# Performance work log

Hardware: AMD Instinct MI355X
Metric: run time of the kernel (lower is better)

The kernel has to match this reference:

```python
import jax, jax.numpy as jnp
import numpy as np

B, N, D, E, H = 8, 256, 128, 32, 4
HD = D // H
EPS = 1e-5


def setup_inputs() -> dict:
    key = jax.random.key(0)
    ks = jax.random.split(key, 20)
    idx = jnp.arange(N)

    h = jax.random.normal(ks[0], (B, N, D), dtype=jnp.float32)
    adj = (jax.random.uniform(ks[1], (B, N, N)) < 0.5).astype(jnp.float32)
    adj = adj.at[:, idx, idx].set(1.0)
    edge_features = jax.random.normal(ks[2], (B, N, N, E), dtype=jnp.float32)
    src_mask = (jax.random.uniform(ks[3], (B, N, N)) < 0.7).astype(jnp.float32)
    src_mask = src_mask.at[:, idx, idx].set(1.0)

    s = 1.0 / np.sqrt(D)
    se = 1.0 / np.sqrt(E)
    p = {
        "gcn_w": jax.random.normal(ks[4], (D, D)) * s,
        "gcn_b": jnp.zeros((D,)),
        "edge_w": jax.random.normal(ks[5], (D, E)) * se,
        "edge_b": jnp.zeros((D,)),
        "wq": jax.random.normal(ks[6], (D, D)) * s,
        "wk": jax.random.normal(ks[7], (D, D)) * s,
        "wv": jax.random.normal(ks[8], (D, D)) * s,
        "bq": jnp.zeros((D,)),
        "bk": jnp.zeros((D,)),
        "bv": jnp.zeros((D,)),
        "out_w": jax.random.normal(ks[9], (D, D)) * s,
        "out_b": jnp.zeros((D,)),
        "ln_g": jnp.ones((D,)),
        "ln_b": jnp.zeros((D,)),
    }
    return {"h": h, "adj": adj, "edge_features": edge_features, "src_mask": src_mask, **p}


def reference(h, adj, edge_features, src_mask,
              gcn_w, gcn_b, edge_w, edge_b,
              wq, wk, wv, bq, bk, bv, out_w, out_b, ln_g, ln_b):
    b, n, d = h.shape

    # --- GCN branch: degree-normalized aggregation with self-loops ---
    adj_sl = adj + jnp.eye(n, dtype=h.dtype)[None]          # (B,N,N)
    deg = adj_sl.sum(-1, keepdims=True)                      # (B,N,1)
    h_agg = jnp.einsum('bnm,bmd->bnd', adj_sl, h) / deg
    h_gcn = h_agg @ gcn_w.T + gcn_b                          # (B,N,D)

    # --- edge-conditioned key/value: h_ij = h_j + edge_emb ---
    edge_emb = jnp.einsum('bnme,de->bnmd', edge_features, edge_w) + edge_b
    h_ij = h[:, None, :, :] + edge_emb                       # (B,N,N,D)

    # key padding mask: True where edge absent (masked)
    masked = (adj * src_mask) == 0                           # (B,N,N)

    # --- multi-head attention, one query per node ---
    q = (h @ wq.T + bq).reshape(b, n, H, HD)                 # (B,N,H,HD)
    k = (jnp.einsum('bnmd,ed->bnme', h_ij, wk) + bk).reshape(b, n, n, H, HD)
    v = (jnp.einsum('bnmd,ed->bnme', h_ij, wv) + bv).reshape(b, n, n, H, HD)

    scores = jnp.einsum('bnhd,bnmhd->bnhm', q, k) / np.sqrt(HD)  # (B,N,H,N)
    scores = jnp.where(masked[:, :, None, :], -jnp.inf, scores)
    attn = jax.nn.softmax(scores, axis=-1)
    o = jnp.einsum('bnhm,bnmhd->bnhd', attn, v).reshape(b, n, d)
    o = o @ out_w.T + out_b                                  # (B,N,D)

    # residual + layernorm (dropout is identity in eval)
    x = h + o
    mu = x.mean(-1, keepdims=True)
    var = ((x - mu) ** 2).mean(-1, keepdims=True)
    h_attn = ln_g * (x - mu) / jnp.sqrt(var + EPS) + ln_b

    return h_gcn + h_attn
```

## Files before the change

### kernel.cpp

```cpp
#include <hip/hip_runtime.h>
#include <hip/hip_bf16.h>

#define OFF_WQT 0
#define OFF_WKT 16384
#define OFF_WVT 32768
#define OFF_OWT 49152
#define OFF_GWT 65536
#define OFF_WKE 81920
#define OFF_WVET 86016
#define OFF_KB  90112
#define OFF_VB  90240
#define OFF_SC  90368
#define OFF_QS  98560
#define OFF_QE  360704
#define OFF_HG  622848
#define OFF_K0  884992
#define OFF_V0  1016064

static __device__ __forceinline__ float bflo(unsigned int w){
  union { unsigned int u; float f; } x; x.u = w << 16; return x.f;
}
static __device__ __forceinline__ float bfhi(unsigned int w){
  union { unsigned int u; float f; } x; x.u = w & 0xffff0000u; return x.f;
}
static __device__ __forceinline__ unsigned int f2bf(float f){
  union { float f; unsigned int u; } x; x.f = f;
  return (x.u + 0x7fffu + ((x.u >> 16) & 1u)) >> 16;
}

__global__ __launch_bounds__(256) void prep_kernel(
    const float* __restrict__ wq, const float* __restrict__ wk,
    const float* __restrict__ wv, const float* __restrict__ out_w,
    const float* __restrict__ gcn_w, const float* __restrict__ edge_w,
    const float* __restrict__ edge_b, const float* __restrict__ bk,
    const float* __restrict__ bv, float* __restrict__ ws)
{
  int blk = blockIdx.x, t = threadIdx.x;
  if (blk < 320) {
    int w = blk >> 6;
    int e0 = (blk & 63) * 256 + t;
    const float* src = (w==0) ? wq : (w==1) ? wk : (w==2) ? wv : (w==3) ? out_w : gcn_w;
    float* dst = ws + ((w==0) ? OFF_WQT : (w==1) ? OFF_WKT : (w==2) ? OFF_WVT
                      : (w==3) ? OFF_OWT : OFF_GWT);
    int k = e0 >> 7, d = e0 & 127;
    dst[e0] = src[d*128 + k];
  } else if (blk < 352) {
    int idx = blk - 320;
    int which = idx >> 4;
    int e0 = (idx & 15) * 256 + t;
    int dd = e0 >> 5, e = e0 & 31;
    const float* W = which ? wv : wk;
    float acc = 0.f;
    #pragma unroll 4
    for (int k2 = 0; k2 < 128; ++k2) acc += W[dd*128+k2] * edge_w[k2*32+e];
    if (which) ws[OFF_WVET + e*128 + dd] = acc;
    else       ws[OFF_WKE + e0] = acc;
  } else {
    int dd = t & 127;
    const float* W  = (t < 128) ? wk : wv;
    const float* bb = (t < 128) ? bk : bv;
    float acc = bb[dd];
    #pragma unroll 4
    for (int k2 = 0; k2 < 128; ++k2) acc += W[dd*128+k2] * edge_b[k2];
    ws[((t < 128) ? OFF_KB : OFF_VB) + dd] = acc;
  }
}

__global__ __launch_bounds__(256) void proj_kernel(
    const float* __restrict__ h, const float* __restrict__ adj,
    const float* __restrict__ bq, const float* __restrict__ gcn_b,
    float* __restrict__ ws)
{
  __shared__ float h_lds[256];
  __shared__ float adj_lds[512];
  __shared__ float p1[2][2][128];
  __shared__ float p2[2][2][128];
  __shared__ float p3[2][2][128];
  __shared__ float qrow[2*132];
  __shared__ float dpart[2][2];
  __shared__ float ha_lds[2*132];

  int t = threadIdx.x;
  int d = t & 127, kh = t >> 7;
  int r0 = blockIdx.x * 2;
  int b  = r0 >> 8, n0 = r0 & 255;

  if (t < 64)  ((float4*)h_lds)[t]   = ((const float4*)(h   + (size_t)r0*128))[t];
  if (t < 128) ((float4*)adj_lds)[t] = ((const float4*)(adj + (size_t)r0*256))[t];
  __syncthreads();

  {
    const float* wqT = ws + OFF_WQT;
    const float* wkT = ws + OFF_WKT;
    const float* wvT = ws + OFF_WVT;
    float aq0=0,aq1=0,ak0=0,ak1=0,av0=0,av1=0;
    #pragma unroll 4
    for (int kk = 0; kk < 64; ++kk) {
      int k = kh*64 + kk;
      float qw = wqT[k*128+d], kw = wkT[k*128+d], vw = wvT[k*128+d];
      float h0 = h_lds[k], h1 = h_lds[128+k];
      aq0 += qw*h0; aq1 += qw*h1;
      ak0 += kw*h0; ak1 += kw*h1;
      av0 += vw*h0; av1 += vw*h1;
    }
    p1[kh][0][d]=aq0; p1[kh][1][d]=aq1;
    p2[kh][0][d]=ak0; p2[kh][1][d]=ak1;
    p3[kh][0][d]=av0; p3[kh][1][d]=av1;
  }
  __syncthreads();

  {
    unsigned short* K0 = (unsigned short*)(ws + OFF_K0);
    unsigned short* V0 = (unsigned short*)(ws + OFF_V0);
    int i = t >> 7, dd = t & 127;
    const float inv = 0.17677669529663687f;
    float q = (p1[0][i][dd] + p1[1][i][dd] + bq[dd]) * inv;
    ws[OFF_QS + (size_t)(r0+i)*128 + dd] = q;
    qrow[i*132 + dd] = q;
    K0[(size_t)(r0+i)*128 + dd] = (unsigned short)f2bf(p2[0][i][dd] + p2[1][i][dd]);
    V0[(size_t)(r0+i)*128 + dd] = (unsigned short)f2bf(p3[0][i][dd] + p3[1][i][dd]);
  }
  __syncthreads();

  {
    float ag0=0, ag1=0, dg0=0, dg1=0;
    #pragma unroll 4
    for (int mm = 0; mm < 128; ++mm) {
      int ml = kh*128 + mm;
      float hv = h[((size_t)b*256 + ml)*128 + d];
      float a0 = adj_lds[ml]       + ((ml == n0)     ? 1.0f : 0.0f);
      float a1 = adj_lds[256 + ml] + ((ml == n0 + 1) ? 1.0f : 0.0f);
      ag0 += a0*hv; ag1 += a1*hv; dg0 += a0; dg1 += a1;
    }
    p1[kh][0][d]=ag0; p1[kh][1][d]=ag1;
    if (d == 0) { dpart[kh][0]=dg0; dpart[kh][1]=dg1; }
  }
  {
    int i = t >> 7, he = t & 127, hh = he >> 5, e = he & 31;
    float acc = 0.f;
    #pragma unroll
    for (int j = 0; j < 32; ++j)
      acc += ws[OFF_WKE + (hh*32 + j)*32 + e] * qrow[i*132 + hh*32 + j];
    ws[OFF_QE + (size_t)(r0+i)*128 + he] = acc;
  }
  if (t < 8) {
    int i = t >> 2, hh = t & 3;
    float acc = 0.f;
    #pragma unroll
    for (int j = 0; j < 32; ++j)
      acc += qrow[i*132 + hh*32 + j] * ws[OFF_KB + hh*32 + j];
    ws[OFF_SC + (size_t)(r0+i)*4 + hh] = acc;
  }
  __syncthreads();

  {
    int i = t >> 7, dd = t & 127;
    ha_lds[i*132 + dd] = (p1[0][i][dd] + p1[1][i][dd]) / (dpart[0][i] + dpart[1][i]);
  }
  __syncthreads();

  {
    const float* gwT = ws + OFF_GWT;
    float g0=0, g1=0;
    #pragma unroll 4
    for (int kk = 0; kk < 64; ++kk) {
      int k = kh*64 + kk;
      float gw = gwT[k*128+d];
      g0 += gw * ha_lds[k];
      g1 += gw * ha_lds[132 + k];
    }
    p2[kh][0][d]=g0; p2[kh][1][d]=g1;
  }
  __syncthreads();
  {
    int i = t >> 7, dd = t & 127;
    ws[OFF_HG + (size_t)(r0+i)*128 + dd] = p2[0][i][dd] + p2[1][i][dd] + gcn_b[dd];
  }
}

__global__ __launch_bounds__(256, 4) void attn_kernel(
    const float* __restrict__ edge, const float* __restrict__ adj,
    const float* __restrict__ srcm, const float* __restrict__ h,
    const float* __restrict__ out_b, const float* __restrict__ ln_g,
    const float* __restrict__ ln_b, const float* __restrict__ ws,
    float* __restrict__ out)
{
  __shared__ unsigned int e_bf[256*18];
  __shared__ float s_lds[4*264];
  __shared__ float part4[8*132];
  __shared__ float part5[8*132];
  __shared__ float qs_l[132];
  __shared__ float qe_l[132];
  __shared__ float sc_l[4];
  __shared__ float ebar[128];
  __shared__ float wpart[16];
  __shared__ float red[2];

  int t  = threadIdx.x;
  int bn = blockIdx.x;
  int b  = bn >> 8;

  {
    const float4* et = (const float4*)(edge + (size_t)bn*8192);
    #pragma unroll
    for (int it = 0; it < 8; ++it) {
      int fi = it*256 + t;
      float4 v = et[fi];
      int row = fi >> 3, c4 = fi & 7;
      uint2 pk;
      pk.x = f2bf(v.x) | (f2bf(v.y) << 16);
      pk.y = f2bf(v.z) | (f2bf(v.w) << 16);
      *(uint2*)(e_bf + row*18 + c4*2) = pk;
    }
    float mp = adj[(size_t)bn*256 + t] * srcm[(size_t)bn*256 + t];
    e_bf[t*18 + 16] = __float_as_uint(mp);
    if (t < 128) {
      int hh = t >> 5, j = t & 31;
      qs_l[hh*33 + j] = ws[OFF_QS + (size_t)bn*128 + t];
      qe_l[hh*33 + j] = ws[OFF_QE + (size_t)bn*128 + t];
    }
    if (t < 4) sc_l[t] = ws[OFF_SC + (size_t)bn*4 + t];
  }
  __syncthreads();

  int hh = t & 3;
  {
    const float* qp  = qs_l + hh*33;
    const float* qep = qe_l + hh*33;
    float exsum = 0.f;
    const unsigned short* K0 = (const unsigned short*)(ws + OFF_K0) + (size_t)b*256*128;
    #pragma unroll 2
    for (int pass = 0; pass < 4; ++pass) {
      int mm = (pass << 6) | (t >> 2);
      const uint4* kv = (const uint4*)(K0 + (size_t)mm*128) + hh*4;
      float acc = sc_l[hh];
      #pragma unroll
      for (int q4 = 0; q4 < 4; ++q4) {
        uint4 kw = kv[q4];
        const float* qq = qp + q4*8;
        acc += qq[0]*bflo(kw.x) + qq[1]*bfhi(kw.x)
             + qq[2]*bflo(kw.y) + qq[3]*bfhi(kw.y)
             + qq[4]*bflo(kw.z) + qq[5]*bfhi(kw.z)
             + qq[6]*bflo(kw.w) + qq[7]*bfhi(kw.w);
      }
      const uint2* er = (const uint2*)(e_bf + mm*18);
      #pragma unroll
      for (int j = 0; j < 8; ++j) {
        uint2 w = er[j];
        acc += qep[4*j+0]*bflo(w.x) + qep[4*j+1]*bfhi(w.x)
             + qep[4*j+2]*bflo(w.y) + qep[4*j+3]*bfhi(w.y);
      }
      float mp = __uint_as_float(e_bf[mm*18 + 16]);
      float ex = (mp == 0.0f) ? 0.0f : __expf(acc);
      s_lds[hh*264 + mm] = ex;
      exsum += ex;
    }
    exsum += __shfl_down(exsum, 4);
    exsum += __shfl_down(exsum, 8);
    exsum += __shfl_down(exsum, 16);
    exsum += __shfl_down(exsum, 32);
    if ((t & 63) < 4) wpart[(t >> 6)*4 + hh] = exsum;
  }
  __syncthreads();

  {
    float s0 = wpart[0]+wpart[4]+wpart[8]+wpart[12];
    float s1 = wpart[1]+wpart[5]+wpart[9]+wpart[13];
    float s2h = wpart[2]+wpart[6]+wpart[10]+wpart[14];
    float s3h = wpart[3]+wpart[7]+wpart[11]+wpart[15];

    int ms  = t >> 5;
    int hh4 = (t >> 3) & 3, e4 = t & 7;
    int c   = t & 31,  hh5 = c >> 3;
    float sum4 = (hh4==0)?s0:(hh4==1)?s1:(hh4==2)?s2h:s3h;
    float sum5 = (hh5==0)?s0:(hh5==1)?s1:(hh5==2)?s2h:s3h;
    float inv4 = 1.0f / sum4, inv5 = 1.0f / sum5;

    float p4x=0,p4y=0,p4z=0,p4w=0;
    float p5x=0,p5y=0,p5z=0,p5w=0;
    const unsigned int* vrow = (const unsigned int*)(ws + OFF_V0) + (size_t)b*256*64;
    for (int jm = 0; jm < 32; ++jm) {
      int mm = ms*32 + jm;
      float a4 = s_lds[hh4*264 + mm];
      uint2 w = *(const uint2*)(e_bf + mm*18 + e4*2);
      p4x += a4*bflo(w.x); p4y += a4*bfhi(w.x);
      p4z += a4*bflo(w.y); p4w += a4*bfhi(w.y);
      float a5 = s_lds[hh5*264 + mm];
      uint2 vv = *(const uint2*)(vrow + (size_t)mm*64 + c*2);
      p5x += a5*bflo(vv.x); p5y += a5*bfhi(vv.x);
      p5z += a5*bflo(vv.y); p5w += a5*bfhi(vv.y);
    }
    float4 f4; f4.x=p4x*inv4; f4.y=p4y*inv4; f4.z=p4z*inv4; f4.w=p4w*inv4;
    *(float4*)(part4 + ms*132 + hh4*32 + e4*4) = f4;
    float4 f5; f5.x=p5x*inv5; f5.y=p5y*inv5; f5.z=p5z*inv5; f5.w=p5w*inv5;
    *(float4*)(part5 + ms*132 + c*4) = f5;
  }
  __syncthreads();

  float s2 = 0.f;
  if (t < 128) {
    float se = 0.f;
    #pragma unroll
    for (int g = 0; g < 8; ++g) { se += part4[g*132 + t]; s2 += part5[g*132 + t]; }
    ebar[t] = se;
  }
  __syncthreads();

  float hv = 0.f;
  if (t < 128) {
    int hd = t >> 5;
    float acc = s2 + ws[OFF_VB + t];
    const float* wveT = ws + OFF_WVET;
    #pragma unroll 4
    for (int e = 0; e < 32; ++e) acc += wveT[e*128 + t] * ebar[hd*32 + e];
    part4[t] = acc;
    hv = h[(size_t)bn*128 + t];
  }
  __syncthreads();

  float x = 0.f;
  if (t < 128) {
    const float* owT = ws + OFF_OWT;
    float acc = out_b[t] + hv;
    #pragma unroll 8
    for (int k = 0; k < 128; ++k) acc += owT[k*128 + t] * part4[k];
    x = acc;
    part4[132 + t] = x;
  }
  __syncthreads();

  if (t < 64) {
    float x0 = part4[132 + t], x1 = part4[132 + t + 64];
    float s = x0 + x1, ss = x0*x0 + x1*x1;
    #pragma unroll
    for (int off = 32; off > 0; off >>= 1) {
      s  += __shfl_down(s,  off);
      ss += __shfl_down(ss, off);
    }
    if (t == 0) {
      float mu = s * (1.0f/128.0f);
      red[0] = mu;
      red[1] = rsqrtf(ss * (1.0f/128.0f) - mu*mu + 1e-5f);
    }
  }
  __syncthreads();

  if (t < 128) {
    float mu = red[0], rs = red[1];
    out[(size_t)bn*128 + t] =
        ln_g[t]*(x - mu)*rs + ln_b[t] + ws[OFF_HG + (size_t)bn*128 + t];
  }
}

extern "C" void kernel_launch(void* const* d_in, const int* in_sizes, int n_in,
                              void* d_out, int out_size, void* d_ws, size_t ws_size,
                              hipStream_t stream) {
  (void)in_sizes; (void)n_in; (void)out_size; (void)ws_size;
  const float* h     = (const float*)d_in[0];
  const float* adj   = (const float*)d_in[1];
  const float* edge  = (const float*)d_in[2];
  const float* srcm  = (const float*)d_in[3];
  const float* gcn_w = (const float*)d_in[4];
  const float* gcn_b = (const float*)d_in[5];
  const float* edge_w= (const float*)d_in[6];
  const float* edge_b= (const float*)d_in[7];
  const float* wq    = (const float*)d_in[8];
  const float* wk    = (const float*)d_in[9];
  const float* wv    = (const float*)d_in[10];
  const float* bq    = (const float*)d_in[11];
  const float* bk    = (const float*)d_in[12];
  const float* bv    = (const float*)d_in[13];
  const float* out_w = (const float*)d_in[14];
  const float* out_b = (const float*)d_in[15];
  const float* ln_g  = (const float*)d_in[16];
  const float* ln_b  = (const float*)d_in[17];

  float* ws  = (float*)d_ws;
  float* out = (float*)d_out;

  prep_kernel<<<353, 256, 0, stream>>>(wq, wk, wv, out_w, gcn_w, edge_w, edge_b, bk, bv, ws);
  proj_kernel<<<1024, 256, 0, stream>>>(h, adj, bq, gcn_b, ws);
  attn_kernel<<<2048, 256, 0, stream>>>(edge, adj, srcm, h, out_b, ln_g, ln_b, ws, out);
}
```

Measured before the change: 189.0 us.

## Tile attention over keys with fp32 K/V and register-prefetched edge features

```diff
diff --git a/kernel.cpp b/kernel.cpp
--- a/kernel.cpp
+++ b/kernel.cpp
@@ -14,19 +14,8 @@
 #define OFF_QS  98560
 #define OFF_QE  360704
 #define OFF_HG  622848
-#define OFF_K0  884992
-#define OFF_V0  1016064
-
-static __device__ __forceinline__ float bflo(unsigned int w){
-  union { unsigned int u; float f; } x; x.u = w << 16; return x.f;
-}
-static __device__ __forceinline__ float bfhi(unsigned int w){
-  union { unsigned int u; float f; } x; x.u = w & 0xffff0000u; return x.f;
-}
-static __device__ __forceinline__ unsigned int f2bf(float f){
-  union { float f; unsigned int u; } x; x.f = f;
-  return (x.u + 0x7fffu + ((x.u >> 16) & 1u)) >> 16;
-}
+#define OFF_KF  884992
+#define OFF_VF  1147136
 
 __global__ __launch_bounds__(256) void prep_kernel(
     const float* __restrict__ wq, const float* __restrict__ wk,
@@ -110,15 +99,13 @@
   __syncthreads();
 
   {
-    unsigned short* K0 = (unsigned short*)(ws + OFF_K0);
-    unsigned short* V0 = (unsigned short*)(ws + OFF_V0);
     int i = t >> 7, dd = t & 127;
     const float inv = 0.17677669529663687f;
     float q = (p1[0][i][dd] + p1[1][i][dd] + bq[dd]) * inv;
     ws[OFF_QS + (size_t)(r0+i)*128 + dd] = q;
     qrow[i*132 + dd] = q;
-    K0[(size_t)(r0+i)*128 + dd] = (unsigned short)f2bf(p2[0][i][dd] + p2[1][i][dd]);
-    V0[(size_t)(r0+i)*128 + dd] = (unsigned short)f2bf(p3[0][i][dd] + p3[1][i][dd]);
+    ws[OFF_KF + (size_t)(r0+i)*128 + dd] = p2[0][i][dd] + p2[1][i][dd];
+    ws[OFF_VF + (size_t)(r0+i)*128 + dd] = p3[0][i][dd] + p3[1][i][dd];
   }
   __syncthreads();
 
@@ -178,142 +165,152 @@
   }
 }
 
-__global__ __launch_bounds__(256, 4) void attn_kernel(
+__global__ __launch_bounds__(256) void attn_kernel(
     const float* __restrict__ edge, const float* __restrict__ adj,
     const float* __restrict__ srcm, const float* __restrict__ h,
     const float* __restrict__ out_b, const float* __restrict__ ln_g,
     const float* __restrict__ ln_b, const float* __restrict__ ws,
     float* __restrict__ out)
 {
-  __shared__ unsigned int e_bf[256*18];
-  __shared__ float s_lds[4*264];
+  __shared__ float e_lds[64*34];
+  __shared__ float s_lds[4*68];
+  __shared__ float mp_lds[256];
+  __shared__ float qs_l[132];
+  __shared__ float sc_l[4];
   __shared__ float part4[8*132];
   __shared__ float part5[8*132];
-  __shared__ float qs_l[132];
-  __shared__ float qe_l[132];
-  __shared__ float sc_l[4];
-  __shared__ float ebar[128];
+  __shared__ float ebar_l[128];
+  __shared__ float o_l[128];
+  __shared__ float x_l[128];
   __shared__ float wpart[16];
   __shared__ float red[2];
 
-  int t  = threadIdx.x;
-  int bn = blockIdx.x;
-  int b  = bn >> 8;
-
-  {
-    const float4* et = (const float4*)(edge + (size_t)bn*8192);
-    #pragma unroll
-    for (int it = 0; it < 8; ++it) {
-      int fi = it*256 + t;
-      float4 v = et[fi];
-      int row = fi >> 3, c4 = fi & 7;
-      uint2 pk;
-      pk.x = f2bf(v.x) | (f2bf(v.y) << 16);
-      pk.y = f2bf(v.z) | (f2bf(v.w) << 16);
-      *(uint2*)(e_bf + row*18 + c4*2) = pk;
-    }
-    float mp = adj[(size_t)bn*256 + t] * srcm[(size_t)bn*256 + t];
-    e_bf[t*18 + 16] = __float_as_uint(mp);
-    if (t < 128) {
-      int hh = t >> 5, j = t & 31;
-      qs_l[hh*33 + j] = ws[OFF_QS + (size_t)bn*128 + t];
-      qe_l[hh*33 + j] = ws[OFF_QE + (size_t)bn*128 + t];
-    }
-    if (t < 4) sc_l[t] = ws[OFF_SC + (size_t)bn*4 + t];
-  }
-  __syncthreads();
-
-  int hh = t & 3;
-  {
-    const float* qp  = qs_l + hh*33;
-    const float* qep = qe_l + hh*33;
-    float exsum = 0.f;
-    const unsigned short* K0 = (const unsigned short*)(ws + OFF_K0) + (size_t)b*256*128;
-    #pragma unroll 2
-    for (int pass = 0; pass < 4; ++pass) {
-      int mm = (pass << 6) | (t >> 2);
-      const uint4* kv = (const uint4*)(K0 + (size_t)mm*128) + hh*4;
+  const int t  = threadIdx.x;
+  const int bn = blockIdx.x;
+  const int b  = bn >> 8;
+  const int hh = t & 3;
+  const int mq = t >> 2;
+  const int c  = t & 31;
+  const int ms = t >> 5;
+
+  float qe_r[4][8];
+  {
+    const float* qeg = ws + OFF_QE + (size_t)bn*128 + hh*8;
+    #pragma unroll
+    for (int hp = 0; hp < 4; ++hp) {
+      float4 a = *(const float4*)(qeg + hp*32);
+      float4 d2 = *(const float4*)(qeg + hp*32 + 4);
+      qe_r[hp][0]=a.x;  qe_r[hp][1]=a.y;  qe_r[hp][2]=a.z;  qe_r[hp][3]=a.w;
+      qe_r[hp][4]=d2.x; qe_r[hp][5]=d2.y; qe_r[hp][6]=d2.z; qe_r[hp][7]=d2.w;
+    }
+  }
+  mp_lds[t] = adj[(size_t)bn*256 + t] * srcm[(size_t)bn*256 + t];
+  if (t < 128) qs_l[(t>>5)*33 + (t&31)] = ws[OFF_QS + (size_t)bn*128 + t];
+  if (t < 4)  sc_l[t] = ws[OFF_SC + (size_t)bn*4 + t];
+
+  const float* eg = edge + (size_t)bn*8192;
+  float4 eA = *(const float4*)(eg + t*8);
+  float4 eB = *(const float4*)(eg + t*8 + 4);
+
+  const float* K0f = ws + OFF_KF + (size_t)b*32768;
+  const float* V0f = ws + OFF_VF + (size_t)b*32768;
+
+  float exacc = 0.f;
+  float p4x=0,p4y=0,p4z=0,p4w=0, p5x=0,p5y=0,p5z=0,p5w=0;
+
+  __syncthreads();
+
+  float4 eA2 = eA, eB2 = eB;
+  for (int tile = 0; tile < 4; ++tile) {
+    {
+      float* dst = e_lds + mq*34 + hh*8;
+      float2 w0; w0.x=eA.x; w0.y=eA.y; *(float2*)(dst+0)=w0;
+      float2 w1; w1.x=eA.z; w1.y=eA.w; *(float2*)(dst+2)=w1;
+      float2 w2; w2.x=eB.x; w2.y=eB.y; *(float2*)(dst+4)=w2;
+      float2 w3; w3.x=eB.z; w3.y=eB.w; *(float2*)(dst+6)=w3;
+    }
+    {
+      const float* qp = qs_l + hh*33;
+      const float4* kv = (const float4*)(K0f + (size_t)(tile*64 + mq)*128 + hh*32);
       float acc = sc_l[hh];
       #pragma unroll
-      for (int q4 = 0; q4 < 4; ++q4) {
-        uint4 kw = kv[q4];
-        const float* qq = qp + q4*8;
-        acc += qq[0]*bflo(kw.x) + qq[1]*bfhi(kw.x)
-             + qq[2]*bflo(kw.y) + qq[3]*bfhi(kw.y)
-             + qq[4]*bflo(kw.z) + qq[5]*bfhi(kw.z)
-             + qq[6]*bflo(kw.w) + qq[7]*bfhi(kw.w);
+      for (int q4 = 0; q4 < 8; ++q4) {
+        float4 kw = kv[q4];
+        const float* qq = qp + q4*4;
+        acc += qq[0]*kw.x + qq[1]*kw.y + qq[2]*kw.z + qq[3]*kw.w;
       }
-      const uint2* er = (const uint2*)(e_bf + mm*18);
-      #pragma unroll
-      for (int j = 0; j < 8; ++j) {
-        uint2 w = er[j];
-        acc += qep[4*j+0]*bflo(w.x) + qep[4*j+1]*bfhi(w.x)
-             + qep[4*j+2]*bflo(w.y) + qep[4*j+3]*bfhi(w.y);
-      }
-      float mp = __uint_as_float(e_bf[mm*18 + 16]);
+      float es0 = eA.x*qe_r[0][0]+eA.y*qe_r[0][1]+eA.z*qe_r[0][2]+eA.w*qe_r[0][3]
+                + eB.x*qe_r[0][4]+eB.y*qe_r[0][5]+eB.z*qe_r[0][6]+eB.w*qe_r[0][7];
+      float es1 = eA.x*qe_r[1][0]+eA.y*qe_r[1][1]+eA.z*qe_r[1][2]+eA.w*qe_r[1][3]
+                + eB.x*qe_r[1][4]+eB.y*qe_r[1][5]+eB.z*qe_r[1][6]+eB.w*qe_r[1][7];
+      float es2 = eA.x*qe_r[2][0]+eA.y*qe_r[2][1]+eA.z*qe_r[2][2]+eA.w*qe_r[2][3]
+                + eB.x*qe_r[2][4]+eB.y*qe_r[2][5]+eB.z*qe_r[2][6]+eB.w*qe_r[2][7];
+      float es3 = eA.x*qe_r[3][0]+eA.y*qe_r[3][1]+eA.z*qe_r[3][2]+eA.w*qe_r[3][3]
+                + eB.x*qe_r[3][4]+eB.y*qe_r[3][5]+eB.z*qe_r[3][6]+eB.w*qe_r[3][7];
+      es0 += __shfl_xor(es0, 1); es0 += __shfl_xor(es0, 2);
+      es1 += __shfl_xor(es1, 1); es1 += __shfl_xor(es1, 2);
+      es2 += __shfl_xor(es2, 1); es2 += __shfl_xor(es2, 2);
+      es3 += __shfl_xor(es3, 1); es3 += __shfl_xor(es3, 2);
+      acc += (hh==0) ? es0 : (hh==1) ? es1 : (hh==2) ? es2 : es3;
+      float mp = mp_lds[tile*64 + mq];
       float ex = (mp == 0.0f) ? 0.0f : __expf(acc);
-      s_lds[hh*264 + mm] = ex;
-      exsum += ex;
-    }
-    exsum += __shfl_down(exsum, 4);
-    exsum += __shfl_down(exsum, 8);
-    exsum += __shfl_down(exsum, 16);
-    exsum += __shfl_down(exsum, 32);
-    if ((t & 63) < 4) wpart[(t >> 6)*4 + hh] = exsum;
-  }
-  __syncthreads();
-
-  {
-    float s0 = wpart[0]+wpart[4]+wpart[8]+wpart[12];
-    float s1 = wpart[1]+wpart[5]+wpart[9]+wpart[13];
-    float s2h = wpart[2]+wpart[6]+wpart[10]+wpart[14];
-    float s3h = wpart[3]+wpart[7]+wpart[11]+wpart[15];
-
-    int ms  = t >> 5;
-    int hh4 = (t >> 3) & 3, e4 = t & 7;
-    int c   = t & 31,  hh5 = c >> 3;
-    float sum4 = (hh4==0)?s0:(hh4==1)?s1:(hh4==2)?s2h:s3h;
-    float sum5 = (hh5==0)?s0:(hh5==1)?s1:(hh5==2)?s2h:s3h;
-    float inv4 = 1.0f / sum4, inv5 = 1.0f / sum5;
-
-    float p4x=0,p4y=0,p4z=0,p4w=0;
-    float p5x=0,p5y=0,p5z=0,p5w=0;
-    const unsigned int* vrow = (const unsigned int*)(ws + OFF_V0) + (size_t)b*256*64;
-    for (int jm = 0; jm < 32; ++jm) {
-      int mm = ms*32 + jm;
-      float a4 = s_lds[hh4*264 + mm];
-      uint2 w = *(const uint2*)(e_bf + mm*18 + e4*2);
-      p4x += a4*bflo(w.x); p4y += a4*bfhi(w.x);
-      p4z += a4*bflo(w.y); p4w += a4*bfhi(w.y);
-      float a5 = s_lds[hh5*264 + mm];
-      uint2 vv = *(const uint2*)(vrow + (size_t)mm*64 + c*2);
-      p5x += a5*bflo(vv.x); p5y += a5*bfhi(vv.x);
-      p5z += a5*bflo(vv.y); p5w += a5*bfhi(vv.y);
-    }
-    float4 f4; f4.x=p4x*inv4; f4.y=p4y*inv4; f4.z=p4z*inv4; f4.w=p4w*inv4;
-    *(float4*)(part4 + ms*132 + hh4*32 + e4*4) = f4;
-    float4 f5; f5.x=p5x*inv5; f5.y=p5y*inv5; f5.z=p5z*inv5; f5.w=p5w*inv5;
+      s_lds[hh*68 + mq] = ex;
+      exacc += ex;
+    }
+    if (tile < 3) {
+      eA2 = *(const float4*)(eg + (tile+1)*2048 + t*8);
+      eB2 = *(const float4*)(eg + (tile+1)*2048 + t*8 + 4);
+    }
+    __syncthreads();
+
+    #pragma unroll
+    for (int jm = 0; jm < 8; ++jm) {
+      int mm = ms*8 + jm;
+      float a = s_lds[(c>>3)*68 + mm];
+      float2 e0 = *(const float2*)(e_lds + mm*34 + (c&7)*4);
+      float2 e1 = *(const float2*)(e_lds + mm*34 + (c&7)*4 + 2);
+      float4 vv = *(const float4*)(V0f + (size_t)(tile*64 + mm)*128 + c*4);
+      p4x += a*e0.x; p4y += a*e0.y; p4z += a*e1.x; p4w += a*e1.y;
+      p5x += a*vv.x; p5y += a*vv.y; p5z += a*vv.z; p5w += a*vv.w;
+    }
+    __syncthreads();
+    eA = eA2; eB = eB2;
+  }
+
+  {
+    float s = exacc;
+    s += __shfl_down(s, 4);  s += __shfl_down(s, 8);
+    s += __shfl_down(s, 16); s += __shfl_down(s, 32);
+    if ((t & 63) < 4) wpart[(t >> 6)*4 + hh] = s;
+  }
+  {
+    float4 f4; f4.x=p4x; f4.y=p4y; f4.z=p4z; f4.w=p4w;
+    *(float4*)(part4 + ms*132 + c*4) = f4;
+    float4 f5; f5.x=p5x; f5.y=p5y; f5.z=p5z; f5.w=p5w;
     *(float4*)(part5 + ms*132 + c*4) = f5;
   }
   __syncthreads();
 
   float s2 = 0.f;
   if (t < 128) {
+    int ht = t >> 5;
+    float inv = 1.0f / (wpart[ht] + wpart[4+ht] + wpart[8+ht] + wpart[12+ht]);
     float se = 0.f;
     #pragma unroll
     for (int g = 0; g < 8; ++g) { se += part4[g*132 + t]; s2 += part5[g*132 + t]; }
-    ebar[t] = se;
+    ebar_l[t] = se * inv;
+    s2 *= inv;
   }
   __syncthreads();
 
   float hv = 0.f;
   if (t < 128) {
-    int hd = t >> 5;
+    int ht = t >> 5;
     float acc = s2 + ws[OFF_VB + t];
     const float* wveT = ws + OFF_WVET;
     #pragma unroll 4
-    for (int e = 0; e < 32; ++e) acc += wveT[e*128 + t] * ebar[hd*32 + e];
-    part4[t] = acc;
+    for (int e = 0; e < 32; ++e) acc += wveT[e*128 + t] * ebar_l[ht*32 + e];
+    o_l[t] = acc;
     hv = h[(size_t)bn*128 + t];
   }
   __syncthreads();
@@ -323,14 +320,14 @@
     const float* owT = ws + OFF_OWT;
     float acc = out_b[t] + hv;
     #pragma unroll 8
-    for (int k = 0; k < 128; ++k) acc += owT[k*128 + t] * part4[k];
+    for (int k = 0; k < 128; ++k) acc += owT[k*128 + t] * o_l[k];
     x = acc;
-    part4[132 + t] = x;
+    x_l[t] = x;
   }
   __syncthreads();
 
   if (t < 64) {
-    float x0 = part4[132 + t], x1 = part4[132 + t + 64];
+    float x0 = x_l[t], x1 = x_l[t + 64];
     float s = x0 + x1, ss = x0*x0 + x1*x1;
     #pragma unroll
     for (int off = 32; off > 0; off >>= 1) {
@@ -346,9 +343,8 @@
   __syncthreads();
 
   if (t < 128) {
-    float mu = red[0], rs = red[1];
     out[(size_t)bn*128 + t] =
-        ln_g[t]*(x - mu)*rs + ln_b[t] + ws[OFF_HG + (size_t)bn*128 + t];
+        ln_g[t]*(x - red[0])*red[1] + ln_b[t] + ws[OFF_HG + (size_t)bn*128 + t];
   }
 }
 
```

After: 258.2 us. +36.6%, slower.

## Switch attention operands to fp16 packed dot2 and split epilogue into batched kernel

Applied to the files above, without the earlier changes.

```diff
diff --git a/kernel.cpp b/kernel.cpp
--- a/kernel.cpp
+++ b/kernel.cpp
@@ -11,21 +11,26 @@
 #define OFF_KB  90112
 #define OFF_VB  90240
 #define OFF_SC  90368
-#define OFF_QS  98560
-#define OFF_QE  360704
-#define OFF_HG  622848
-#define OFF_K0  884992
-#define OFF_V0  1016064
-
-static __device__ __forceinline__ float bflo(unsigned int w){
-  union { unsigned int u; float f; } x; x.u = w << 16; return x.f;
-}
-static __device__ __forceinline__ float bfhi(unsigned int w){
-  union { unsigned int u; float f; } x; x.u = w & 0xffff0000u; return x.f;
-}
-static __device__ __forceinline__ unsigned int f2bf(float f){
-  union { float f; unsigned int u; } x; x.f = f;
-  return (x.u + 0x7fffu + ((x.u >> 16) & 1u)) >> 16;
+#define OFF_QSP 98560
+#define OFF_QEP 229632
+#define OFF_HG  360704
+#define OFF_EB  622848
+#define OFF_OV  884992
+#define OFF_K0P 1147136
+#define OFF_V0P 1278208
+
+using half2_t = __attribute__((ext_vector_type(2))) __fp16;
+
+static __device__ __forceinline__ half2_t u2h(unsigned int u){
+  union { unsigned int u; half2_t h; } x; x.u = u; return x.h;
+}
+static __device__ __forceinline__ unsigned int pkf16(float a, float b){
+  union { half2_t h; unsigned int u; } x;
+  x.h = __builtin_amdgcn_cvt_pkrtz(a, b);
+  return x.u;
+}
+static __device__ __forceinline__ float fdot2(unsigned int a, unsigned int b, float c){
+  return __builtin_amdgcn_fdot2(u2h(a), u2h(b), c, false);
 }
 
 __global__ __launch_bounds__(256) void prep_kernel(
@@ -77,6 +82,7 @@
   __shared__ float p2[2][2][128];
   __shared__ float p3[2][2][128];
   __shared__ float qrow[2*132];
+  __shared__ float qe_l[2*132];
   __shared__ float dpart[2][2];
   __shared__ float ha_lds[2*132];
 
@@ -84,6 +90,7 @@
   int d = t & 127, kh = t >> 7;
   int r0 = blockIdx.x * 2;
   int b  = r0 >> 8, n0 = r0 & 255;
+  unsigned int* wsu = (unsigned int*)ws;
 
   if (t < 64)  ((float4*)h_lds)[t]   = ((const float4*)(h   + (size_t)r0*128))[t];
   if (t < 128) ((float4*)adj_lds)[t] = ((const float4*)(adj + (size_t)r0*256))[t];
@@ -110,18 +117,44 @@
   __syncthreads();
 
   {
-    unsigned short* K0 = (unsigned short*)(ws + OFF_K0);
-    unsigned short* V0 = (unsigned short*)(ws + OFF_V0);
     int i = t >> 7, dd = t & 127;
     const float inv = 0.17677669529663687f;
-    float q = (p1[0][i][dd] + p1[1][i][dd] + bq[dd]) * inv;
-    ws[OFF_QS + (size_t)(r0+i)*128 + dd] = q;
-    qrow[i*132 + dd] = q;
-    K0[(size_t)(r0+i)*128 + dd] = (unsigned short)f2bf(p2[0][i][dd] + p2[1][i][dd]);
-    V0[(size_t)(r0+i)*128 + dd] = (unsigned short)f2bf(p3[0][i][dd] + p3[1][i][dd]);
-  }
-  __syncthreads();
-
+    qrow[i*132 + dd] = (p1[0][i][dd] + p1[1][i][dd] + bq[dd]) * inv;
+  }
+  {
+    int i = (t >> 6) & 1, pr = t & 63;
+    if (t < 128) {
+      float k0 = p2[0][i][2*pr] + p2[1][i][2*pr];
+      float k1 = p2[0][i][2*pr+1] + p2[1][i][2*pr+1];
+      wsu[OFF_K0P + (size_t)(r0+i)*64 + pr] = pkf16(k0, k1);
+    } else {
+      float v0 = p3[0][i][2*pr] + p3[1][i][2*pr];
+      float v1 = p3[0][i][2*pr+1] + p3[1][i][2*pr+1];
+      wsu[OFF_V0P + (size_t)(r0+i)*64 + pr] = pkf16(v0, v1);
+    }
+  }
+  __syncthreads();
+
+  if (t < 128) {
+    int i = t >> 6, pr = t & 63;
+    wsu[OFF_QSP + (size_t)(r0+i)*64 + pr] = pkf16(qrow[i*132 + 2*pr], qrow[i*132 + 2*pr+1]);
+  }
+  {
+    int i = t >> 7, he = t & 127, hh = he >> 5, e = he & 31;
+    float acc = 0.f;
+    #pragma unroll
+    for (int j = 0; j < 32; ++j)
+      acc += ws[OFF_WKE + (hh*32 + j)*32 + e] * qrow[i*132 + hh*32 + j];
+    qe_l[i*132 + he] = acc;
+  }
+  if (t < 8) {
+    int i = t >> 2, hh = t & 3;
+    float acc = 0.f;
+    #pragma unroll
+    for (int j = 0; j < 32; ++j)
+      acc += qrow[i*132 + hh*32 + j] * ws[OFF_KB + hh*32 + j];
+    ws[OFF_SC + (size_t)(r0+i)*4 + hh] = acc;
+  }
   {
     float ag0=0, ag1=0, dg0=0, dg1=0;
     #pragma unroll 4
@@ -135,24 +168,12 @@
     p1[kh][0][d]=ag0; p1[kh][1][d]=ag1;
     if (d == 0) { dpart[kh][0]=dg0; dpart[kh][1]=dg1; }
   }
-  {
-    int i = t >> 7, he = t & 127, hh = he >> 5, e = he & 31;
-    float acc = 0.f;
-    #pragma unroll
-    for (int j = 0; j < 32; ++j)
-      acc += ws[OFF_WKE + (hh*32 + j)*32 + e] * qrow[i*132 + hh*32 + j];
-    ws[OFF_QE + (size_t)(r0+i)*128 + he] = acc;
-  }
-  if (t < 8) {
-    int i = t >> 2, hh = t & 3;
-    float acc = 0.f;
-    #pragma unroll
-    for (int j = 0; j < 32; ++j)
-      acc += qrow[i*132 + hh*32 + j] * ws[OFF_KB + hh*32 + j];
-    ws[OFF_SC + (size_t)(r0+i)*4 + hh] = acc;
-  }
-  __syncthreads();
-
+  __syncthreads();
+
+  if (t < 128) {
+    int i = t >> 6, pr = t & 63;
+    wsu[OFF_QEP + (size_t)(r0+i)*64 + pr] = pkf16(qe_l[i*132 + 2*pr], qe_l[i*132 + 2*pr+1]);
+  }
   {
     int i = t >> 7, dd = t & 127;
     ha_lds[i*132 + dd] = (p1[0][i][dd] + p1[1][i][dd]) / (dpart[0][i] + dpart[1][i]);
@@ -180,25 +201,21 @@
 
 __global__ __launch_bounds__(256, 4) void attn_kernel(
     const float* __restrict__ edge, const float* __restrict__ adj,
-    const float* __restrict__ srcm, const float* __restrict__ h,
-    const float* __restrict__ out_b, const float* __restrict__ ln_g,
-    const float* __restrict__ ln_b, const float* __restrict__ ws,
-    float* __restrict__ out)
+    const float* __restrict__ srcm, const float* __restrict__ ws,
+    float* __restrict__ dummy)
 {
-  __shared__ unsigned int e_bf[256*18];
+  __shared__ unsigned int e_lds[256*18];
   __shared__ float s_lds[4*264];
   __shared__ float part4[8*132];
   __shared__ float part5[8*132];
-  __shared__ float qs_l[132];
-  __shared__ float qe_l[132];
-  __shared__ float sc_l[4];
-  __shared__ float ebar[128];
   __shared__ float wpart[16];
-  __shared__ float red[2];
-
-  int t  = threadIdx.x;
-  int bn = blockIdx.x;
-  int b  = bn >> 8;
+
+  const int t  = threadIdx.x;
+  const int bn = blockIdx.x;
+  const int b  = bn >> 8;
+  const int hh = t & 3;
+  const int mq = t >> 2;
+  const unsigned int* wsu = (const unsigned int*)ws;
 
   {
     const float4* et = (const float4*)(edge + (size_t)bn*8192);
@@ -208,147 +225,184 @@
       float4 v = et[fi];
       int row = fi >> 3, c4 = fi & 7;
       uint2 pk;
-      pk.x = f2bf(v.x) | (f2bf(v.y) << 16);
-      pk.y = f2bf(v.z) | (f2bf(v.w) << 16);
-      *(uint2*)(e_bf + row*18 + c4*2) = pk;
+      pk.x = pkf16(v.x, v.y);
+      pk.y = pkf16(v.z, v.w);
+      *(uint2*)(e_lds + row*18 + c4*2) = pk;
     }
     float mp = adj[(size_t)bn*256 + t] * srcm[(size_t)bn*256 + t];
-    e_bf[t*18 + 16] = __float_as_uint(mp);
-    if (t < 128) {
-      int hh = t >> 5, j = t & 31;
-      qs_l[hh*33 + j] = ws[OFF_QS + (size_t)bn*128 + t];
-      qe_l[hh*33 + j] = ws[OFF_QE + (size_t)bn*128 + t];
-    }
-    if (t < 4) sc_l[t] = ws[OFF_SC + (size_t)bn*4 + t];
-  }
-  __syncthreads();
-
-  int hh = t & 3;
-  {
-    const float* qp  = qs_l + hh*33;
-    const float* qep = qe_l + hh*33;
-    float exsum = 0.f;
-    const unsigned short* K0 = (const unsigned short*)(ws + OFF_K0) + (size_t)b*256*128;
-    #pragma unroll 2
+    e_lds[t*18 + 16] = __float_as_uint(mp);
+  }
+  unsigned int qs_pk[16], qe_pk[16];
+  {
+    const uint4* qp = (const uint4*)(wsu + OFF_QSP + (size_t)bn*64 + hh*16);
+    const uint4* qe = (const uint4*)(wsu + OFF_QEP + (size_t)bn*64 + hh*16);
+    #pragma unroll
+    for (int j = 0; j < 4; ++j) {
+      uint4 a = qp[j];
+      qs_pk[4*j+0]=a.x; qs_pk[4*j+1]=a.y; qs_pk[4*j+2]=a.z; qs_pk[4*j+3]=a.w;
+      uint4 c = qe[j];
+      qe_pk[4*j+0]=c.x; qe_pk[4*j+1]=c.y; qe_pk[4*j+2]=c.z; qe_pk[4*j+3]=c.w;
+    }
+  }
+  float sconst = ws[OFF_SC + (size_t)bn*4 + hh];
+  __syncthreads();
+
+  float exacc = 0.f;
+  {
+    const unsigned int* K0 = wsu + OFF_K0P + (size_t)b*256*64;
     for (int pass = 0; pass < 4; ++pass) {
-      int mm = (pass << 6) | (t >> 2);
-      const uint4* kv = (const uint4*)(K0 + (size_t)mm*128) + hh*4;
-      float acc = sc_l[hh];
+      int mm = (pass << 6) | mq;
+      float acc = sconst;
+      const uint4* kr4 = (const uint4*)(K0 + (size_t)mm*64 + hh*16);
       #pragma unroll
-      for (int q4 = 0; q4 < 4; ++q4) {
-        uint4 kw = kv[q4];
-        const float* qq = qp + q4*8;
-        acc += qq[0]*bflo(kw.x) + qq[1]*bfhi(kw.x)
-             + qq[2]*bflo(kw.y) + qq[3]*bfhi(kw.y)
-             + qq[4]*bflo(kw.z) + qq[5]*bfhi(kw.z)
-             + qq[6]*bflo(kw.w) + qq[7]*bfhi(kw.w);
+      for (int j4 = 0; j4 < 4; ++j4) {
+        uint4 kw = kr4[j4];
+        acc = fdot2(qs_pk[4*j4+0], kw.x, acc);
+        acc = fdot2(qs_pk[4*j4+1], kw.y, acc);
+        acc = fdot2(qs_pk[4*j4+2], kw.z, acc);
+        acc = fdot2(qs_pk[4*j4+3], kw.w, acc);
       }
-      const uint2* er = (const uint2*)(e_bf + mm*18);
+      const uint2* er = (const uint2*)(e_lds + mm*18);
       #pragma unroll
-      for (int j = 0; j < 8; ++j) {
-        uint2 w = er[j];
-        acc += qep[4*j+0]*bflo(w.x) + qep[4*j+1]*bfhi(w.x)
-             + qep[4*j+2]*bflo(w.y) + qep[4*j+3]*bfhi(w.y);
+      for (int j2 = 0; j2 < 8; ++j2) {
+        uint2 w = er[j2];
+        acc = fdot2(qe_pk[2*j2+0], w.x, acc);
+        acc = fdot2(qe_pk[2*j2+1], w.y, acc);
       }
-      float mp = __uint_as_float(e_bf[mm*18 + 16]);
+      float mp = __uint_as_float(e_lds[mm*18 + 16]);
       float ex = (mp == 0.0f) ? 0.0f : __expf(acc);
       s_lds[hh*264 + mm] = ex;
-      exsum += ex;
-    }
-    exsum += __shfl_down(exsum, 4);
-    exsum += __shfl_down(exsum, 8);
-    exsum += __shfl_down(exsum, 16);
-    exsum += __shfl_down(exsum, 32);
-    if ((t & 63) < 4) wpart[(t >> 6)*4 + hh] = exsum;
-  }
-  __syncthreads();
-
-  {
-    float s0 = wpart[0]+wpart[4]+wpart[8]+wpart[12];
-    float s1 = wpart[1]+wpart[5]+wpart[9]+wpart[13];
-    float s2h = wpart[2]+wpart[6]+wpart[10]+wpart[14];
-    float s3h = wpart[3]+wpart[7]+wpart[11]+wpart[15];
-
+      exacc += ex;
+    }
+    exacc += __shfl_down(exacc, 4);
+    exacc += __shfl_down(exacc, 8);
+    exacc += __shfl_down(exacc, 16);
+    exacc += __shfl_down(exacc, 32);
+    if ((t & 63) < 4) wpart[(t >> 6)*4 + hh] = exacc;
+  }
+  __syncthreads();
+
+  {
     int ms  = t >> 5;
     int hh4 = (t >> 3) & 3, e4 = t & 7;
     int c   = t & 31,  hh5 = c >> 3;
-    float sum4 = (hh4==0)?s0:(hh4==1)?s1:(hh4==2)?s2h:s3h;
-    float sum5 = (hh5==0)?s0:(hh5==1)?s1:(hh5==2)?s2h:s3h;
-    float inv4 = 1.0f / sum4, inv5 = 1.0f / sum5;
-
     float p4x=0,p4y=0,p4z=0,p4w=0;
     float p5x=0,p5y=0,p5z=0,p5w=0;
-    const unsigned int* vrow = (const unsigned int*)(ws + OFF_V0) + (size_t)b*256*64;
+    const unsigned int* vrow = wsu + OFF_V0P + (size_t)b*256*64;
     for (int jm = 0; jm < 32; ++jm) {
       int mm = ms*32 + jm;
       float a4 = s_lds[hh4*264 + mm];
-      uint2 w = *(const uint2*)(e_bf + mm*18 + e4*2);
-      p4x += a4*bflo(w.x); p4y += a4*bfhi(w.x);
-      p4z += a4*bflo(w.y); p4w += a4*bfhi(w.y);
+      uint2 w = *(const uint2*)(e_lds + mm*18 + e4*2);
+      half2_t e0 = u2h(w.x), e1 = u2h(w.y);
+      p4x += a4*(float)e0.x; p4y += a4*(float)e0.y;
+      p4z += a4*(float)e1.x; p4w += a4*(float)e1.y;
       float a5 = s_lds[hh5*264 + mm];
       uint2 vv = *(const uint2*)(vrow + (size_t)mm*64 + c*2);
-      p5x += a5*bflo(vv.x); p5y += a5*bfhi(vv.x);
-      p5z += a5*bflo(vv.y); p5w += a5*bfhi(vv.y);
-    }
-    float4 f4; f4.x=p4x*inv4; f4.y=p4y*inv4; f4.z=p4z*inv4; f4.w=p4w*inv4;
+      half2_t v0 = u2h(vv.x), v1 = u2h(vv.y);
+      p5x += a5*(float)v0.x; p5y += a5*(float)v0.y;
+      p5z += a5*(float)v1.x; p5w += a5*(float)v1.y;
+    }
+    float4 f4; f4.x=p4x; f4.y=p4y; f4.z=p4z; f4.w=p4w;
     *(float4*)(part4 + ms*132 + hh4*32 + e4*4) = f4;
-    float4 f5; f5.x=p5x*inv5; f5.y=p5y*inv5; f5.z=p5z*inv5; f5.w=p5w*inv5;
+    float4 f5; f5.x=p5x; f5.y=p5y; f5.z=p5z; f5.w=p5w;
     *(float4*)(part5 + ms*132 + c*4) = f5;
   }
   __syncthreads();
 
-  float s2 = 0.f;
   if (t < 128) {
-    float se = 0.f;
+    int ht = t >> 5;
+    float inv = 1.0f / (wpart[ht] + wpart[4+ht] + wpart[8+ht] + wpart[12+ht]);
+    float se = 0.f, s2 = 0.f;
     #pragma unroll
     for (int g = 0; g < 8; ++g) { se += part4[g*132 + t]; s2 += part5[g*132 + t]; }
-    ebar[t] = se;
-  }
-  __syncthreads();
-
-  float hv = 0.f;
-  if (t < 128) {
-    int hd = t >> 5;
-    float acc = s2 + ws[OFF_VB + t];
+    float* wso = (float*)ws;
+    wso[OFF_EB + (size_t)bn*128 + t] = se * inv;
+    wso[OFF_OV + (size_t)bn*128 + t] = s2 * inv;
+  }
+  (void)dummy;
+}
+
+__global__ __launch_bounds__(256) void epi_kernel(
+    const float* __restrict__ h, const float* __restrict__ out_b,
+    const float* __restrict__ ln_g, const float* __restrict__ ln_b,
+    const float* __restrict__ ws, float* __restrict__ out)
+{
+  __shared__ float eb_l[4*132];
+  __shared__ float o_l[4*132];
+  __shared__ float xl[4*132];
+  __shared__ float pp[2][4][128];
+  __shared__ float stat[8];
+
+  int t = threadIdx.x;
+  int d = t & 127, kh = t >> 7;
+  int r0 = blockIdx.x * 4;
+
+  #pragma unroll
+  for (int rep = 0; rep < 2; ++rep) {
+    int idx = rep*256 + t, i = idx >> 7, dd = idx & 127;
+    eb_l[i*132 + dd] = ws[OFF_EB + (size_t)(r0+i)*128 + dd];
+  }
+  __syncthreads();
+
+  #pragma unroll
+  for (int rep = 0; rep < 2; ++rep) {
+    int idx = rep*256 + t, i = idx >> 7, dd = idx & 127;
+    int hd = dd >> 5;
+    float acc = ws[OFF_OV + (size_t)(r0+i)*128 + dd] + ws[OFF_VB + dd];
     const float* wveT = ws + OFF_WVET;
     #pragma unroll 4
-    for (int e = 0; e < 32; ++e) acc += wveT[e*128 + t] * ebar[hd*32 + e];
-    part4[t] = acc;
-    hv = h[(size_t)bn*128 + t];
-  }
-  __syncthreads();
-
-  float x = 0.f;
-  if (t < 128) {
+    for (int e = 0; e < 32; ++e) acc += wveT[e*128 + dd] * eb_l[i*132 + hd*32 + e];
+    o_l[i*132 + dd] = acc;
+  }
+  __syncthreads();
+
+  {
     const float* owT = ws + OFF_OWT;
-    float acc = out_b[t] + hv;
-    #pragma unroll 8
-    for (int k = 0; k < 128; ++k) acc += owT[k*128 + t] * part4[k];
-    x = acc;
-    part4[132 + t] = x;
-  }
-  __syncthreads();
-
-  if (t < 64) {
-    float x0 = part4[132 + t], x1 = part4[132 + t + 64];
+    float xa[4] = {0,0,0,0};
+    #pragma unroll 4
+    for (int kk = 0; kk < 64; ++kk) {
+      int k = kh*64 + kk;
+      float ow = owT[k*128 + d];
+      #pragma unroll
+      for (int i = 0; i < 4; ++i) xa[i] += ow * o_l[i*132 + k];
+    }
+    #pragma unroll
+    for (int i = 0; i < 4; ++i) pp[kh][i][d] = xa[i];
+  }
+  __syncthreads();
+
+  #pragma unroll
+  for (int rep = 0; rep < 2; ++rep) {
+    int idx = rep*256 + t, i = idx >> 7, dd = idx & 127;
+    xl[i*132 + dd] = pp[0][i][dd] + pp[1][i][dd] + out_b[dd]
+                   + h[(size_t)(r0+i)*128 + dd];
+  }
+  __syncthreads();
+
+  {
+    int i = t >> 6, l = t & 63;
+    float x0 = xl[i*132 + l], x1 = xl[i*132 + l + 64];
     float s = x0 + x1, ss = x0*x0 + x1*x1;
     #pragma unroll
     for (int off = 32; off > 0; off >>= 1) {
       s  += __shfl_down(s,  off);
       ss += __shfl_down(ss, off);
     }
-    if (t == 0) {
-      float mu = s * (1.0f/128.0f);
-      red[0] = mu;
-      red[1] = rsqrtf(ss * (1.0f/128.0f) - mu*mu + 1e-5f);
-    }
-  }
-  __syncthreads();
-
-  if (t < 128) {
-    float mu = red[0], rs = red[1];
-    out[(size_t)bn*128 + t] =
-        ln_g[t]*(x - mu)*rs + ln_b[t] + ws[OFF_HG + (size_t)bn*128 + t];
+    if (l == 0) {
+      float mu  = s * (1.0f/128.0f);
+      float var = ss * (1.0f/128.0f) - mu*mu;
+      stat[i]   = mu;
+      stat[4+i] = rsqrtf(var + 1e-5f);
+    }
+  }
+  __syncthreads();
+
+  #pragma unroll
+  for (int rep = 0; rep < 2; ++rep) {
+    int idx = rep*256 + t, i = idx >> 7, dd = idx & 127;
+    float x = xl[i*132 + dd];
+    out[(size_t)(r0+i)*128 + dd] =
+        ln_g[dd]*(x - stat[i])*stat[4+i] + ln_b[dd] + ws[OFF_HG + (size_t)(r0+i)*128 + dd];
   }
 }
 
@@ -380,5 +434,6 @@
 
   prep_kernel<<<353, 256, 0, stream>>>(wq, wk, wv, out_w, gcn_w, edge_w, edge_b, bk, bv, ws);
   proj_kernel<<<1024, 256, 0, stream>>>(h, adj, bq, gcn_b, ws);
-  attn_kernel<<<2048, 256, 0, stream>>>(edge, adj, srcm, h, out_b, ln_g, ln_b, ws, out);
-}
+  attn_kernel<<<2048, 256, 0, stream>>>(edge, adj, srcm, ws, out);
+  epi_kernel<<<512, 256, 0, stream>>>(h, out_b, ln_g, ln_b, ws, out);
+}
```

After: 188.5 us (median of 2 runs). Within noise of the previous version (-0.3%).
